# Kernel optimization log

Hardware: AMD Instinct MI355X
Metric: run time of the kernel (lower is better)

The kernel has to match this reference:

```python
import jax, jax.numpy as jnp
import numpy as np

B, S, E, H = 2, 2048, 1024, 16
D = E // H  # head_dim = 64


def setup_inputs() -> dict:
    key = jax.random.key(0)
    k1, k2, k3 = jax.random.split(key, 3)
    scale_in = 1.0 / np.sqrt(E)
    return {
        "x": jax.random.normal(k1, (B, S, E), dtype=jnp.float32),
        "mask": jnp.ones((B, S), dtype=jnp.int32),
        "qkv_w": jax.random.normal(k2, (3 * E, E), dtype=jnp.float32) * scale_in,
        "qkv_b": jnp.zeros((3 * E,), dtype=jnp.float32),
        "proj_w": jax.random.normal(k3, (E, E), dtype=jnp.float32) * scale_in,
        "proj_b": jnp.zeros((E,), dtype=jnp.float32),
    }


def reference(x, mask, qkv_w, qkv_b, proj_w, proj_b):
    b, s, e = x.shape
    # fused QKV projection: torch Linear -> x @ W^T + b
    qkv = x @ qkv_w.T + qkv_b                      # [B,S,3E]
    qkv = qkv.reshape(b, s, 3, H, D).transpose(2, 0, 3, 1, 4)  # [3,B,H,S,D]
    q, k, v = qkv[0], qkv[1], qkv[2]
    scores = jnp.einsum("bhqd,bhkd->bhqk", q, k) / jnp.sqrt(jnp.float32(D))
    # mask [B,S] -> [B,1,1,S]; masked_fill(mask==0, -inf)
    m = mask[:, None, None, :]
    scores = jnp.where(m == 0, -jnp.inf, scores)
    attn = jax.nn.softmax(scores, axis=-1)
    attn = jnp.nan_to_num(attn, nan=0.0)           # fully-masked rows -> 0
    # dropout is identity in eval mode (deterministic reference)
    out = jnp.einsum("bhqk,bhkd->bhqd", attn, v)   # [B,H,S,D]
    out = out.transpose(0, 2, 1, 3).reshape(b, s, e)
    out = out @ proj_w.T + proj_b
    return out
```

## Files before the change

### kernel.cpp

```cpp
#include <hip/hip_runtime.h>
#include <hip/hip_bf16.h>

#define B_ 2
#define S_ 2048
#define E_ 1024
#define H_ 16
#define D_ 64

typedef __bf16 bf16x8 __attribute__((ext_vector_type(8)));
typedef __bf16 bf16x4 __attribute__((ext_vector_type(4)));
typedef float f32x4 __attribute__((ext_vector_type(4)));


__device__ __forceinline__ f32x4 mfma16(bf16x8 a, bf16x8 b, f32x4 c) {
    return __builtin_amdgcn_mfma_f32_16x16x32_bf16(a, b, c, 0, 0, 0);
}

__device__ __forceinline__ void gl_lds16(const __bf16* g, __bf16* l) {
    __builtin_amdgcn_global_load_lds(
        (const __attribute__((address_space(1))) unsigned int*)g,
        (__attribute__((address_space(3))) unsigned int*)l, 16, 0, 0);
}
__device__ __forceinline__ void gl_lds4(const int* g, int* l) {
    __builtin_amdgcn_global_load_lds(
        (const __attribute__((address_space(1))) unsigned int*)g,
        (__attribute__((address_space(3))) unsigned int*)l, 4, 0, 0);
}

__global__ __launch_bounds__(256) void convert_kernel(
        const float* __restrict__ x, const float* __restrict__ qkvw,
        const float* __restrict__ projw, __bf16* __restrict__ ws) {
    const long NX = 4194304, NW = 3145728;
    long i = (long)(blockIdx.x * 256 + threadIdx.x) * 4;
    const float* src; __bf16* dst; long off;
    if (i < NX)           { src = x;     dst = ws;           off = i; }
    else if (i < NX + NW) { src = qkvw;  dst = ws + NX;      off = i - NX; }
    else                  { src = projw; dst = ws + NX + NW; off = i - NX - NW; }
    float4 v = *(const float4*)(src + off);
    bf16x4 o = { (__bf16)v.x, (__bf16)v.y, (__bf16)v.z, (__bf16)v.w };
    *(bf16x4*)(dst + off) = o;
}

__device__ __forceinline__ void gemm_core(
        const __bf16* __restrict__ A, const __bf16* __restrict__ Bm,
        int rowT, int colT, int K,
        __bf16* AT, __bf16* BT, f32x4 acc[4][4]) {
    int tid = threadIdx.x;
    int wave = tid >> 6, lane = tid & 63;
    int quad = lane >> 4, lm = lane & 15;
    int wy = wave >> 1, wx = wave & 1;
    int srow = wave * 8 + (lane >> 3);
    int schunk = lane & 7;
    const __bf16* ap = A + (long)(rowT + srow) * K + schunk * 8;
    const __bf16* bp = Bm + (long)(colT + srow) * K + schunk * 8;
    for (int k0 = 0; k0 < K; k0 += 64) {
        __syncthreads();
        for (int i = 0; i < 4; i++) {
            gl_lds16(ap + (long)i * 32 * K + k0, AT + (i * 256 + wave * 64) * 8);
            gl_lds16(bp + (long)i * 32 * K + k0, BT + (i * 256 + wave * 64) * 8);
        }
        __syncthreads();
        for (int ks = 0; ks < 2; ks++) {
            bf16x8 af[4], bfr[4];
            for (int m = 0; m < 4; m++)
                af[m] = *(const bf16x8*)(AT + (wy * 64 + m * 16 + lm) * 64 + ks * 32 + quad * 8);
            for (int n = 0; n < 4; n++)
                bfr[n] = *(const bf16x8*)(BT + (wx * 64 + n * 16 + lm) * 64 + ks * 32 + quad * 8);
            for (int m = 0; m < 4; m++)
                for (int n = 0; n < 4; n++)
                    acc[m][n] = mfma16(af[m], bfr[n], acc[m][n]);
        }
    }
}

__device__ __forceinline__ void gemm_core_h(
        const __bf16* __restrict__ A, const __bf16* __restrict__ Bm,
        int rowT, int colT, int K,
        __bf16* AT, __bf16* BT, f32x4 acc[2][4]) {
    int tid = threadIdx.x;
    int wave = tid >> 6, lane = tid & 63;
    int quad = lane >> 4, lm = lane & 15;
    int srow = wave * 8 + (lane >> 3);
    int schunk = lane & 7;
    const __bf16* ap = A + (long)(rowT + srow) * K + schunk * 8;
    const __bf16* bp = Bm + (long)(colT + srow) * K + schunk * 8;
    for (int k0 = 0; k0 < K; k0 += 64) {
        __syncthreads();
        for (int i = 0; i < 4; i++)
            gl_lds16(ap + (long)i * 32 * K + k0, AT + (i * 256 + wave * 64) * 8);
        for (int i = 0; i < 2; i++)
            gl_lds16(bp + (long)i * 32 * K + k0, BT + (i * 256 + wave * 64) * 8);
        __syncthreads();
        for (int ks = 0; ks < 2; ks++) {
            bf16x8 af[2], bfr[4];
            for (int m = 0; m < 2; m++)
                af[m] = *(const bf16x8*)(AT + (wave * 32 + m * 16 + lm) * 64 + ks * 32 + quad * 8);
            for (int n = 0; n < 4; n++)
                bfr[n] = *(const bf16x8*)(BT + (n * 16 + lm) * 64 + ks * 32 + quad * 8);
            for (int m = 0; m < 2; m++)
                for (int n = 0; n < 4; n++)
                    acc[m][n] = mfma16(af[m], bfr[n], acc[m][n]);
        }
    }
}

#define C1 0.18033688011112043f

__global__ __launch_bounds__(256, 3) void qkv_gemm(
        const __bf16* __restrict__ xbf, const __bf16* __restrict__ wbf,
        const float* __restrict__ bias, __bf16* __restrict__ qk,
        __bf16* __restrict__ vt) {
    __shared__ __align__(16) __bf16 AT[128 * 64];
    __shared__ __align__(16) __bf16 BT[128 * 64];
    f32x4 acc[4][4] = {};
    int rowT = blockIdx.x * 128, colT = blockIdx.y * 128;
    gemm_core(xbf, wbf, rowT, colT, E_, AT, BT, acc);
    int wave = threadIdx.x >> 6, lane = threadIdx.x & 63;
    int quad = lane >> 4, lm = lane & 15;
    int wy = wave >> 1, wx = wave & 1;
    int which = colT >> 10;
    if (which < 2) {
        float sc = which ? 1.f : C1;
        for (int n = 0; n < 4; n++) {
            int col = colT + wx * 64 + n * 16 + lm;
            float bv = bias[col];
            int rem = col & 1023;
            int h = rem >> 6, d = rem & 63;
            for (int m = 0; m < 4; m++) {
                int rowb = rowT + wy * 64 + m * 16 + quad * 4;
                for (int r = 0; r < 4; r++) {
                    int row = rowb + r;
                    int b = row >> 11, s = row & 2047;
                    float v = (acc[m][n][r] + bv) * sc;
                    qk[(long)((which * B_ + b) * H_ + h) * (S_ * D_) + (long)s * D_ + d] = (__bf16)v;
                }
            }
        }
    } else {
        for (int n = 0; n < 4; n++) {
            int col = colT + wx * 64 + n * 16 + lm;
            float bv = bias[col];
            int mr = col & 1023;
            int h = mr >> 6, d = mr & 63;
            for (int m = 0; m < 4; m++) {
                int row = rowT + wy * 64 + m * 16 + quad * 4;
                int b = row >> 11, s = row & 2047;
                bf16x4 o = { (__bf16)(acc[m][n][0] + bv), (__bf16)(acc[m][n][1] + bv),
                             (__bf16)(acc[m][n][2] + bv), (__bf16)(acc[m][n][3] + bv) };
                *(bf16x4*)(vt + (long)((b * H_ + h) * D_ + d) * S_ + s) = o;
            }
        }
    }
}

__global__ __launch_bounds__(256, 3) void flash_attn(
        const __bf16* __restrict__ qk, const __bf16* __restrict__ vt,
        const int* __restrict__ mask, __bf16* __restrict__ attn) {
    int wave = threadIdx.x >> 6, lane = threadIdx.x & 63;
    int quad = lane >> 4, lm = lane & 15;
    int bh = blockIdx.x;
    int qb = blockIdx.y;
    int b = bh >> 4, h = bh & 15;
    const long BHSD = (long)B_ * H_ * S_ * D_;
    const __bf16* qp  = qk + (long)bh * (S_ * D_);
    const __bf16* kp  = qk + BHSD + (long)bh * (S_ * D_);
    const __bf16* vtp = vt + (long)bh * (D_ * S_);
    const int* mrow = mask + b * S_;

    __shared__ __align__(16) __bf16 Kl[2][64 * 64];
    __shared__ __align__(16) __bf16 Vl[2][64 * 64];
    __shared__ __align__(16) int    Ml[2][64];
    __shared__ __align__(16) __bf16 Plds[4][2][16][72];

    int q0[2];
    q0[0] = qb * 128 + wave * 32;
    q0[1] = q0[0] + 16;
    bf16x8 qa[2][2];
    for (int t = 0; t < 2; t++)
        for (int x = 0; x < 2; x++)
            qa[t][x] = *(const bf16x8*)(qp + (long)(q0[t] + lm) * D_ + x * 32 + quad * 8);

    f32x4 O[2][4] = {};
    f32x4 Ol[2] = {};
    bf16x8 ones8;
    for (int j = 0; j < 8; j++) ones8[j] = (__bf16)1.0f;
    const f32x4 zinit = {-32.f, -32.f, -32.f, -32.f};

    struct __align__(8) bfx4 { __hip_bfloat162 lo, hi; };

    int r8 = lane >> 3, c8 = lane & 7;
    int cs = c8 ^ r8;
    int xs = lm & 7;

    {
        for (int j = 0; j < 2; j++) {
            int wp = wave * 2 + j;
            int row = wp * 8 + r8;
            gl_lds16(kp + (long)row * 64 + cs * 8, &Kl[0][wp * 512]);
            gl_lds16(vtp + (long)row * S_ + cs * 8, &Vl[0][wp * 512]);
        }
        if (wave == 0) gl_lds4(mrow + lane, &Ml[0][0]);
    }
    __syncthreads();

    for (int i = 0; i < 32; i++) {
        int bs = i & 1;
        if (i < 31) {
            int kb1 = (i + 1) * 64;
            #pragma unroll
            for (int j = 0; j < 2; j++) {
                int wp = wave * 2 + j;
                int row = wp * 8 + r8;
                gl_lds16(kp + (long)(kb1 + row) * 64 + cs * 8, &Kl[bs ^ 1][wp * 512]);
                gl_lds16(vtp + (long)row * S_ + kb1 + cs * 8, &Vl[bs ^ 1][wp * 512]);
            }
            if (wave == 0) gl_lds4(mrow + kb1 + lane, &Ml[bs ^ 1][0]);
        }
        const __bf16* Kb = &Kl[bs][0];
        #pragma unroll
        for (int g = 0; g < 2; g++) {
            bf16x8 kf[2][2];
            int4 mq[2];
            #pragma unroll
            for (int j = 0; j < 2; j++) {
                int hh = g * 2 + j;
                int row = hh * 16 + lm;
                kf[j][0] = *(const bf16x8*)(Kb + row * 64 + ((quad ^ xs) << 3));
                kf[j][1] = *(const bf16x8*)(Kb + row * 64 + (((4 + quad) ^ xs) << 3));
                mq[j] = *(const int4*)(&Ml[bs][hh * 16 + quad * 4]);
            }
            f32x4 st[2][2];
            __builtin_amdgcn_s_setprio(1);
            #pragma unroll
            for (int j = 0; j < 2; j++)
                #pragma unroll
                for (int t = 0; t < 2; t++) {
                    f32x4 z = mfma16(kf[j][0], qa[t][0], zinit);
                    st[j][t] = mfma16(kf[j][1], qa[t][1], z);
                }
            __builtin_amdgcn_s_setprio(0);
            #pragma unroll
            for (int j = 0; j < 2; j++)
                #pragma unroll
                for (int t = 0; t < 2; t++) {
                    int hh = g * 2 + j;
                    float e0 = __builtin_amdgcn_exp2f(mq[j].x ? st[j][t][0] : -1e38f);
                    float e1 = __builtin_amdgcn_exp2f(mq[j].y ? st[j][t][1] : -1e38f);
                    float e2 = __builtin_amdgcn_exp2f(mq[j].z ? st[j][t][2] : -1e38f);
                    float e3 = __builtin_amdgcn_exp2f(mq[j].w ? st[j][t][3] : -1e38f);
                    bfx4 pk;
                    pk.lo = __float22bfloat162_rn(float2{e0, e1});
                    pk.hi = __float22bfloat162_rn(float2{e2, e3});
                    *(bfx4*)(&Plds[wave][t][lm][hh * 16 + quad * 4]) = pk;
                }
        }
        const __bf16* Vb = &Vl[bs][0];
        bf16x8 vf[2][4];
        #pragma unroll
        for (int x = 0; x < 2; x++)
            #pragma unroll
            for (int c = 0; c < 4; c++) {
                int row = c * 16 + lm;
                vf[x][c] = *(const bf16x8*)(Vb + row * 64 + ((((x << 2) + quad) ^ xs) << 3));
            }
        bf16x8 pa[2][2];
        #pragma unroll
        for (int x = 0; x < 2; x++)
            #pragma unroll
            for (int t = 0; t < 2; t++)
                pa[x][t] = *(const bf16x8*)(&Plds[wave][t][lm][x * 32 + quad * 8]);
        __builtin_amdgcn_s_setprio(1);
        #pragma unroll
        for (int x = 0; x < 2; x++)
            #pragma unroll
            for (int t = 0; t < 2; t++) {
                #pragma unroll
                for (int c = 0; c < 4; c++)
                    O[t][c] = mfma16(pa[x][t], vf[x][c], O[t][c]);
                Ol[t] = mfma16(pa[x][t], ones8, Ol[t]);
            }
        __builtin_amdgcn_s_setprio(0);
        __syncthreads();
    }

    for (int t = 0; t < 2; t++)
        for (int r = 0; r < 4; r++) {
            float lb = Ol[t][r];
            float inv = lb > 0.f ? 1.f / lb : 0.f;
            int s = q0[t] + quad * 4 + r;
            for (int c = 0; c < 4; c++) {
                int e = h * 64 + c * 16 + lm;
                attn[(long)(b * S_ + s) * E_ + e] = (__bf16)(O[t][c][r] * inv);
            }
        }
}

__global__ __launch_bounds__(256, 2) void proj_gemm(
        const __bf16* __restrict__ abf, const __bf16* __restrict__ wbf,
        const float* __restrict__ bias, float* __restrict__ out) {
    __shared__ __align__(16) __bf16 AT[128 * 64];
    __shared__ __align__(16) __bf16 BT[64 * 64];
    f32x4 acc[2][4] = {};
    int rowT = blockIdx.x * 128, colT = blockIdx.y * 64;
    gemm_core_h(abf, wbf, rowT, colT, E_, AT, BT, acc);
    int wave = threadIdx.x >> 6, lane = threadIdx.x & 63;
    int quad = lane >> 4, lm = lane & 15;
    for (int n = 0; n < 4; n++) {
        int col = colT + n * 16 + lm;
        float bv = bias[col];
        for (int m = 0; m < 2; m++) {
            int rowb = rowT + wave * 32 + m * 16 + quad * 4;
            for (int r = 0; r < 4; r++) {
                int row = rowb + r;
                out[(long)row * E_ + col] = acc[m][n][r] + bv;
            }
        }
    }
}

extern "C" void kernel_launch(void* const* d_in, const int* in_sizes, int n_in,
                              void* d_out, int out_size, void* d_ws, size_t ws_size,
                              hipStream_t stream) {
    const float* x      = (const float*)d_in[0];
    const int*   mask   = (const int*)d_in[1];
    const float* qkv_w  = (const float*)d_in[2];
    const float* qkv_b  = (const float*)d_in[3];
    const float* proj_w = (const float*)d_in[4];
    const float* proj_b = (const float*)d_in[5];
    float* out = (float*)d_out;
    __bf16* ws = (__bf16*)d_ws;

    __bf16* x_bf     = ws;
    __bf16* qkvw_bf  = ws + 4194304;
    __bf16* projw_bf = ws + 7340032;
    __bf16* qk_bf    = ws + 8388608;
    __bf16* vt_bf    = ws + 16777216;
    __bf16* attn_bf  = ws + 20971520;

    convert_kernel<<<8192, 256, 0, stream>>>(x, qkv_w, proj_w, ws);
    qkv_gemm<<<dim3(32, 24), 256, 0, stream>>>(x_bf, qkvw_bf, qkv_b, qk_bf, vt_bf);
    flash_attn<<<dim3(32, 16), 256, 0, stream>>>(qk_bf, vt_bf, mask, attn_bf);
    proj_gemm<<<dim3(32, 16), 256, 0, stream>>>(attn_bf, projw_bf, proj_b, out);
}
```

Baseline: 187.4 us.

## Enlarge flash attention blocks to 8 waves with 128-key tiles

The flash attention kernel now runs 512 threads per block covering 256 query rows, and each iteration stages 128 keys instead of 64. The grid is halved along the query axis and the loop count is halved. Each K/V tile loaded into LDS is now shared by twice as many waves, and there are half as many barriers per key. The V tile gets a new 16-way XOR swizzle for the 128-wide rows. In exchange the kernel uses more LDS per block and launches fewer blocks (256 instead of 512), which can lower occupancy and the number of CUs kept busy.

```diff
diff --git a/kernel.cpp b/kernel.cpp
--- a/kernel.cpp
+++ b/kernel.cpp
@@ -153,7 +153,7 @@
     }
 }
 
-__global__ __launch_bounds__(256, 3) void flash_attn(
+__global__ __launch_bounds__(512, 2) void flash_attn(
         const __bf16* __restrict__ qk, const __bf16* __restrict__ vt,
         const int* __restrict__ mask, __bf16* __restrict__ attn) {
     int wave = threadIdx.x >> 6, lane = threadIdx.x & 63;
@@ -167,13 +167,13 @@
     const __bf16* vtp = vt + (long)bh * (D_ * S_);
     const int* mrow = mask + b * S_;
 
-    __shared__ __align__(16) __bf16 Kl[2][64 * 64];
-    __shared__ __align__(16) __bf16 Vl[2][64 * 64];
-    __shared__ __align__(16) int    Ml[2][64];
-    __shared__ __align__(16) __bf16 Plds[4][2][16][72];
+    __shared__ __align__(16) __bf16 Kl[2][128 * 64];
+    __shared__ __align__(16) __bf16 Vl[2][64 * 128];
+    __shared__ __align__(16) int    Ml[2][128];
+    __shared__ __align__(16) __bf16 Plds[8][2][16][136];
 
     int q0[2];
-    q0[0] = qb * 128 + wave * 32;
+    q0[0] = qb * 256 + wave * 32;
     q0[1] = q0[0] + 16;
     bf16x8 qa[2][2];
     for (int t = 0; t < 2; t++)
@@ -193,32 +193,43 @@
     int xs = lm & 7;
 
     {
+        #pragma unroll
         for (int j = 0; j < 2; j++) {
             int wp = wave * 2 + j;
-            int row = wp * 8 + r8;
-            gl_lds16(kp + (long)row * 64 + cs * 8, &Kl[0][wp * 512]);
-            gl_lds16(vtp + (long)row * S_ + cs * 8, &Vl[0][wp * 512]);
-        }
-        if (wave == 0) gl_lds4(mrow + lane, &Ml[0][0]);
+            int krow = wp * 8 + r8;
+            gl_lds16(kp + (long)krow * 64 + cs * 8, &Kl[0][wp * 512]);
+            int vrow = wp * 4 + quad;
+            int vcs = lm ^ (vrow & 15);
+            gl_lds16(vtp + (long)vrow * S_ + vcs * 8, &Vl[0][wp * 512]);
+        }
+        if (wave == 0) {
+            gl_lds4(mrow + lane, &Ml[0][0]);
+            gl_lds4(mrow + 64 + lane, &Ml[0][64]);
+        }
     }
     __syncthreads();
 
-    for (int i = 0; i < 32; i++) {
+    for (int i = 0; i < 16; i++) {
         int bs = i & 1;
-        if (i < 31) {
-            int kb1 = (i + 1) * 64;
+        if (i < 15) {
+            int kb1 = (i + 1) * 128;
             #pragma unroll
             for (int j = 0; j < 2; j++) {
                 int wp = wave * 2 + j;
-                int row = wp * 8 + r8;
-                gl_lds16(kp + (long)(kb1 + row) * 64 + cs * 8, &Kl[bs ^ 1][wp * 512]);
-                gl_lds16(vtp + (long)row * S_ + kb1 + cs * 8, &Vl[bs ^ 1][wp * 512]);
-            }
-            if (wave == 0) gl_lds4(mrow + kb1 + lane, &Ml[bs ^ 1][0]);
+                int krow = wp * 8 + r8;
+                gl_lds16(kp + (long)(kb1 + krow) * 64 + cs * 8, &Kl[bs ^ 1][wp * 512]);
+                int vrow = wp * 4 + quad;
+                int vcs = lm ^ (vrow & 15);
+                gl_lds16(vtp + (long)vrow * S_ + kb1 + vcs * 8, &Vl[bs ^ 1][wp * 512]);
+            }
+            if (wave == 0) {
+                gl_lds4(mrow + kb1 + lane, &Ml[bs ^ 1][0]);
+                gl_lds4(mrow + kb1 + 64 + lane, &Ml[bs ^ 1][64]);
+            }
         }
         const __bf16* Kb = &Kl[bs][0];
         #pragma unroll
-        for (int g = 0; g < 2; g++) {
+        for (int g = 0; g < 4; g++) {
             bf16x8 kf[2][2];
             int4 mq[2];
             #pragma unroll
@@ -255,31 +266,28 @@
                 }
         }
         const __bf16* Vb = &Vl[bs][0];
-        bf16x8 vf[2][4];
         #pragma unroll
-        for (int x = 0; x < 2; x++)
+        for (int x = 0; x < 4; x++) {
+            bf16x8 vf[4];
             #pragma unroll
             for (int c = 0; c < 4; c++) {
                 int row = c * 16 + lm;
-                vf[x][c] = *(const bf16x8*)(Vb + row * 64 + ((((x << 2) + quad) ^ xs) << 3));
-            }
-        bf16x8 pa[2][2];
-        #pragma unroll
-        for (int x = 0; x < 2; x++)
+                vf[c] = *(const bf16x8*)(Vb + row * 128 + (((x * 4 + quad) ^ lm) << 3));
+            }
+            bf16x8 pa[2];
             #pragma unroll
             for (int t = 0; t < 2; t++)
-                pa[x][t] = *(const bf16x8*)(&Plds[wave][t][lm][x * 32 + quad * 8]);
-        __builtin_amdgcn_s_setprio(1);
-        #pragma unroll
-        for (int x = 0; x < 2; x++)
+                pa[t] = *(const bf16x8*)(&Plds[wave][t][lm][x * 32 + quad * 8]);
+            __builtin_amdgcn_s_setprio(1);
             #pragma unroll
             for (int t = 0; t < 2; t++) {
                 #pragma unroll
                 for (int c = 0; c < 4; c++)
-                    O[t][c] = mfma16(pa[x][t], vf[x][c], O[t][c]);
-                Ol[t] = mfma16(pa[x][t], ones8, Ol[t]);
-            }
-        __builtin_amdgcn_s_setprio(0);
+                    O[t][c] = mfma16(pa[t], vf[c], O[t][c]);
+                Ol[t] = mfma16(pa[t], ones8, Ol[t]);
+            }
+            __builtin_amdgcn_s_setprio(0);
+        }
         __syncthreads();
     }
 
@@ -339,6 +347,6 @@
 
     convert_kernel<<<8192, 256, 0, stream>>>(x, qkv_w, proj_w, ws);
     qkv_gemm<<<dim3(32, 24), 256, 0, stream>>>(x_bf, qkvw_bf, qkv_b, qk_bf, vt_bf);
-    flash_attn<<<dim3(32, 16), 256, 0, stream>>>(qk_bf, vt_bf, mask, attn_bf);
+    flash_attn<<<dim3(32, 8), 512, 0, stream>>>(qk_bf, vt_bf, mask, attn_bf);
     proj_gemm<<<dim3(32, 16), 256, 0, stream>>>(attn_bf, projw_bf, proj_b, out);
 }
```

Measured after the change: 186.7 us. About the same (-0.4%).
